# Kernel optimization log

Measured on AMD Instinct MI355X. Metric: run time of the kernel, lower is better.

## Reference

```python
import jax, jax.numpy as jnp
import numpy as np

NUM_HEADS = 4
CATEGORY_SIZE = 128
DIM = 192
B, N, M = 2, 65000, 64


def setup_inputs() -> dict:
    key = jax.random.key(0)
    k1, k2, k3, k4 = jax.random.split(key, 4)
    qkv = jax.random.normal(k1, (B, N, 3 * DIM), dtype=jnp.float32)
    sim = jax.random.normal(k2, (B, N, M), dtype=jnp.float32)
    proj_w = jax.random.normal(k3, (DIM, DIM), dtype=jnp.float32) * (1.0 / np.sqrt(DIM))
    proj_b = jax.random.normal(k4, (DIM,), dtype=jnp.float32) * 0.01
    logit_scale = jnp.log(10.0 * jnp.ones((1, 1), dtype=jnp.float32))
    return {"qkv": qkv, "sim": sim, "proj_w": proj_w, "proj_b": proj_b,
            "logit_scale": logit_scale, "x_size": 65000}


def reference(qkv, sim, proj_w, proj_b, logit_scale, x_size):
    b, n, c3 = qkv.shape
    c = c3 // 3
    h = NUM_HEADS
    gs = min(n, CATEGORY_SIZE)
    ng = (n + gs - 1) // gs
    pad_n = ng * gs - n

    # token -> category id, then sort tokens by category
    tk_id = jnp.argmax(sim, axis=-1)                      # (b, n) int
    sort_idx = jnp.argsort(tk_id, axis=-1)                # (b, n)
    inv_idx = jnp.argsort(sort_idx, axis=-1)              # inverse permutation

    shuffled = jnp.take_along_axis(qkv, sort_idx[..., None], axis=1)  # (b, n, 3c)
    if pad_n > 0:
        pad = jnp.flip(shuffled[:, n - pad_n:n, :], axis=1)
        shuffled = jnp.concatenate([shuffled, pad], axis=1)           # (b, n+pad_n, 3c)

    # (3, b, ng, h, gs, c/h)
    y = shuffled.reshape(b, ng, gs, 3, h, c // h).transpose(3, 0, 1, 4, 2, 5)
    q, k, v = y[0], y[1], y[2]

    scale = jnp.exp(jnp.minimum(logit_scale, jnp.log(jnp.asarray(100.0, dtype=qkv.dtype))))
    attn = jnp.einsum('bghqd,bghkd->bghqk', q, k) * scale  # (b, ng, h, gs, gs)
    attn = jax.nn.softmax(attn, axis=-1)
    out = jnp.einsum('bghqk,bghkd->bghqd', attn, v)        # (b, ng, h, gs, c/h)
    out = out.transpose(0, 1, 3, 2, 4).reshape(b, n + pad_n, c)[:, :n, :]

    # scatter back to original token order
    out = jnp.take_along_axis(out, inv_idx[..., None], axis=1)
    return out @ proj_w.T + proj_b
```

## Files before the change

### kernel.cpp

```cpp
#include <hip/hip_runtime.h>
#include <hip/hip_bf16.h>
#include <math.h>

#define BB 2
#define NN 65000
#define MM 64
#define DIM 192
#define NH 4
#define HD 48
#define GS 128
#define NG 508
#define SORT_TPB 256
#define NBLK 254

#define NROWS_PAD 130048
#define NROWTILES 2032

typedef __attribute__((ext_vector_type(8))) short bf16x8;
typedef __attribute__((ext_vector_type(8))) _Float16 f16x8;
typedef __attribute__((ext_vector_type(2))) __fp16 fp16x2;
typedef __attribute__((ext_vector_type(4))) float f32x4;
typedef __attribute__((ext_vector_type(16))) float f32x16;
typedef __attribute__((ext_vector_type(8))) unsigned short u16x8;

__device__ __forceinline__ unsigned short f2bf(float f) {
  __hip_bfloat16 h = __float2bfloat16(f);
  return *(unsigned short*)&h;
}
__device__ __forceinline__ unsigned int pkh(float lo, float hi) {
  fp16x2 t = __builtin_amdgcn_cvt_pkrtz(lo, hi);
  return *(unsigned int*)&t;
}
__device__ __forceinline__ f16x8 cvt8h(float4 a, float4 b) {
  f16x8 r;
  r[0] = (_Float16)a.x; r[1] = (_Float16)a.y; r[2] = (_Float16)a.z; r[3] = (_Float16)a.w;
  r[4] = (_Float16)b.x; r[5] = (_Float16)b.y; r[6] = (_Float16)b.z; r[7] = (_Float16)b.w;
  return r;
}
__device__ __forceinline__ void gload_lds16(const float* src, float* lds_dst) {
  __builtin_amdgcn_global_load_lds(
      (const __attribute__((address_space(1))) unsigned int*)src,
      (__attribute__((address_space(3))) unsigned int*)lds_dst, 16, 0, 0);
}

__global__ void k_argmax_hist(const float* __restrict__ sim, int* __restrict__ tk,
                              int* __restrict__ hist) {
  __shared__ int cnt[MM];
  const int b = blockIdx.y, blk = blockIdx.x;
  if (threadIdx.x < MM) cnt[threadIdx.x] = 0;
  __syncthreads();
  int t = blk * SORT_TPB + threadIdx.x;
  if (t < NN) {
    const float4* row = (const float4*)(sim + ((size_t)b * NN + t) * MM);
    float best = -INFINITY;
    int bi = 0;
#pragma unroll
    for (int j = 0; j < MM / 4; ++j) {
      float4 v = row[j];
      if (v.x > best) { best = v.x; bi = 4 * j + 0; }
      if (v.y > best) { best = v.y; bi = 4 * j + 1; }
      if (v.z > best) { best = v.z; bi = 4 * j + 2; }
      if (v.w > best) { best = v.w; bi = 4 * j + 3; }
    }
    tk[b * NN + t] = bi;
    atomicAdd(&cnt[bi], 1);
  }
  __syncthreads();
  if (threadIdx.x < MM)
    hist[(b * NBLK + blk) * MM + threadIdx.x] = cnt[threadIdx.x];
}

__global__ void k_scan(const int* __restrict__ hist, int* __restrict__ boff) {
  const int b = blockIdx.x;
  const int tid = threadIdx.x;
  const int seg = tid >> 6, bin = tid & 63;
  __shared__ int part[4][MM];
  __shared__ int basev[MM];
  const int lo = seg * 64, hi = (seg == 3) ? NBLK : (lo + 64);
  int s = 0;
  for (int blk = lo; blk < hi; ++blk) s += hist[(b * NBLK + blk) * MM + bin];
  part[seg][bin] = s;
  __syncthreads();
  if (tid < 64) {
    int tot = part[0][bin] + part[1][bin] + part[2][bin] + part[3][bin];
    int incl = tot;
#pragma unroll
    for (int d = 1; d < 64; d <<= 1) {
      int o = __shfl_up(incl, d);
      if (bin >= d) incl += o;
    }
    basev[bin] = incl - tot;
  }
  __syncthreads();
  int run = basev[bin];
  for (int s2 = 0; s2 < seg; ++s2) run += part[s2][bin];
  for (int blk = lo; blk < hi; ++blk) {
    int h = hist[(b * NBLK + blk) * MM + bin];
    boff[(b * NBLK + blk) * MM + bin] = run;
    run += h;
  }
}

__global__ void k_scatter(const int* __restrict__ tk, const int* __restrict__ boff,
                          int* __restrict__ sidx) {
  __shared__ int sbin[SORT_TPB];
  const int b = blockIdx.y, blk = blockIdx.x;
  int t = blk * SORT_TPB + threadIdx.x;
  int bin = (t < NN) ? tk[b * NN + t] : -1;
  sbin[threadIdx.x] = bin;
  __syncthreads();
  if (t < NN) {
    int rank = 0;
    for (int j = 0; j < (int)threadIdx.x; ++j) rank += (sbin[j] == bin);
    int pos = boff[(b * NBLK + blk) * MM + bin] + rank;
    sidx[b * NN + pos] = t;
  }
}

__global__ __launch_bounds__(256) void k_attn_mfma(const float* __restrict__ qkv,
                                                   const int* __restrict__ sidx,
                                                   const float* __restrict__ logit_scale,
                                                   __hip_bfloat16* __restrict__ attn_out) {
  const int x = blockIdx.x;
  const int g = ((x >> 5) << 3) + (x & 7);
  const int hd = (x >> 3) & 3;
  const int b = blockIdx.z;
  if (g >= NG) return;

  __shared__ int stok[GS];
  __shared__ _Float16 akv[4 * 3 * 64 * 8];
  __shared__ float vrowf[GS][HD];
  __shared__ _Float16 vfrag[2 * 8 * 64 * 8];

  const int tid = threadIdx.x;
  const int w = tid >> 6, l = tid & 63;
  const int hl = l >> 5, l31 = l & 31;

  if (tid < GS) {
    int s = g * GS + tid;
    int sp = (s < NN) ? s : (2 * NN - 1 - s);
    stok[tid] = sidx[b * NN + sp];
  }
  __syncthreads();

#pragma unroll
  for (int i = 0; i < 6; ++i) {
    int c = (i * 4 + w) * 64 + l;
    int row = c / 12, piece = c % 12;
    const float* src = qkv + (size_t)(b * NN + stok[row]) * (3 * DIM) + 2 * DIM + hd * HD + piece * 4;
    gload_lds16(src, &vrowf[0][0] + (i * 4 + w) * 256);
  }

  f16x8 qf[3];
  {
    const float* qsrc = qkv + (size_t)(b * NN + stok[w * 32 + l31]) * (3 * DIM) + hd * HD;
#pragma unroll
    for (int s = 0; s < 3; ++s) {
      const float4* p = (const float4*)(qsrc + s * 16 + hl * 8);
      qf[s] = cvt8h(p[0], p[1]);
    }
  }

#pragma unroll
  for (int i = 0; i < 3; ++i) {
    int c = tid + 256 * i;
    int ts = c >> 6, cl = c & 63;
    int kvr = (ts / 3) * 32 + (cl & 31);
    int dbase = (ts % 3) * 16 + (cl >> 5) * 8;
    const float* src = qkv + (size_t)(b * NN + stok[kvr]) * (3 * DIM) + DIM + hd * HD + dbase;
    ((f16x8*)akv)[c] = cvt8h(((const float4*)src)[0], ((const float4*)src)[1]);
  }
  __syncthreads();

#pragma unroll
  for (int i = 0; i < 4; ++i) {
    int c = tid + 256 * i;
    int ntks = c >> 6, cl = c & 63;
    int nt = ntks >> 3, ks = ntks & 7;
    int d = nt * 32 + (cl & 31);
    int kvb = ks * 16 + (cl >> 5) * 8;
    _Float16 tmp[8];
#pragma unroll
    for (int e = 0; e < 8; ++e) tmp[e] = (d < HD) ? (_Float16)vrowf[kvb + e][d] : (_Float16)0.f;
    ((f16x8*)vfrag)[c] = *(f16x8*)tmp;
  }
  __syncthreads();

  f32x16 accS[4];
#pragma unroll
  for (int t = 0; t < 4; ++t)
#pragma unroll
    for (int r = 0; r < 16; ++r) accS[t][r] = 0.f;

#pragma unroll
  for (int t = 0; t < 4; ++t)
#pragma unroll
    for (int s = 0; s < 3; ++s) {
      f16x8 af = ((const f16x8*)akv)[(t * 3 + s) * 64 + l];
      accS[t] = __builtin_amdgcn_mfma_f32_32x32x16_f16(af, qf[s], accS[t], 0, 0, 0);
    }

  const float scale = expf(fminf(logit_scale[0], 4.6051701860f));
  float mx = -INFINITY;
#pragma unroll
  for (int t = 0; t < 4; ++t)
#pragma unroll
    for (int r = 0; r < 16; ++r) { accS[t][r] *= scale; mx = fmaxf(mx, accS[t][r]); }
  mx = fmaxf(mx, __shfl_xor(mx, 32));
  float sum = 0.f;
#pragma unroll
  for (int t = 0; t < 4; ++t)
#pragma unroll
    for (int r = 0; r < 16; ++r) { float p = __expf(accS[t][r] - mx); accS[t][r] = p; sum += p; }
  sum += __shfl_xor(sum, 32);
  const float inv = 1.f / sum;
#pragma unroll
  for (int t = 0; t < 4; ++t)
#pragma unroll
    for (int r = 0; r < 16; ++r) accS[t][r] *= inv;

  f32x16 accO[2];
#pragma unroll
  for (int nt = 0; nt < 2; ++nt)
#pragma unroll
    for (int r = 0; r < 16; ++r) accO[nt][r] = 0.f;

#pragma unroll
  for (int t = 0; t < 4; ++t) {
    union { unsigned int u[4]; f16x8 v; } fa, fb;
    {
      unsigned int a0 = pkh(accS[t][0], accS[t][1]);
      unsigned int a1 = pkh(accS[t][2], accS[t][3]);
      unsigned int b0 = pkh(accS[t][4], accS[t][5]);
      unsigned int b1 = pkh(accS[t][6], accS[t][7]);
      unsigned int sa0 = __shfl_xor(a0, 32), sa1 = __shfl_xor(a1, 32);
      unsigned int sb0 = __shfl_xor(b0, 32), sb1 = __shfl_xor(b1, 32);
      fa.u[0] = hl ? sb0 : a0; fa.u[1] = hl ? sb1 : a1;
      fa.u[2] = hl ? b0 : sa0; fa.u[3] = hl ? b1 : sa1;
    }
    {
      unsigned int a0 = pkh(accS[t][8], accS[t][9]);
      unsigned int a1 = pkh(accS[t][10], accS[t][11]);
      unsigned int b0 = pkh(accS[t][12], accS[t][13]);
      unsigned int b1 = pkh(accS[t][14], accS[t][15]);
      unsigned int sa0 = __shfl_xor(a0, 32), sa1 = __shfl_xor(a1, 32);
      unsigned int sb0 = __shfl_xor(b0, 32), sb1 = __shfl_xor(b1, 32);
      fb.u[0] = hl ? sb0 : a0; fb.u[1] = hl ? sb1 : a1;
      fb.u[2] = hl ? b0 : sa0; fb.u[3] = hl ? b1 : sa1;
    }
    accO[0] = __builtin_amdgcn_mfma_f32_32x32x16_f16(fa.v, ((const f16x8*)vfrag)[(0 * 8 + 2 * t) * 64 + l], accO[0], 0, 0, 0);
    accO[1] = __builtin_amdgcn_mfma_f32_32x32x16_f16(fa.v, ((const f16x8*)vfrag)[(1 * 8 + 2 * t) * 64 + l], accO[1], 0, 0, 0);
    accO[0] = __builtin_amdgcn_mfma_f32_32x32x16_f16(fb.v, ((const f16x8*)vfrag)[(0 * 8 + 2 * t + 1) * 64 + l], accO[0], 0, 0, 0);
    accO[1] = __builtin_amdgcn_mfma_f32_32x32x16_f16(fb.v, ((const f16x8*)vfrag)[(1 * 8 + 2 * t + 1) * 64 + l], accO[1], 0, 0, 0);
  }

#pragma unroll
  for (int r = 0; r < 16; ++r) {
    int rowl = w * 32 + (r & 3) + 8 * (r >> 2) + 4 * hl;
    int sg = g * GS + rowl;
    if (sg < NN) {
      size_t base = (size_t)(b * NN + stok[rowl]) * DIM + hd * HD;
      attn_out[base + l31] = __float2bfloat16(accO[0][r]);
      if (l31 < 16) attn_out[base + 32 + l31] = __float2bfloat16(accO[1][r]);
    }
  }
}

__global__ void k_wpack(const float* __restrict__ W, unsigned short* __restrict__ wpack) {
  int idx = blockIdx.x * blockDim.x + threadIdx.x;
  if (idx >= 12 * 6 * 64) return;
  int lane = idx & 63;
  int kkjt = idx >> 6;
  int kk = kkjt % 6;
  int jt = kkjt / 6;
  int j = jt * 16 + (lane & 15);
  int k0 = kk * 32 + (lane >> 4) * 8;
  const float* src = W + (size_t)j * DIM + k0;
  unsigned short tmp[8];
#pragma unroll
  for (int e = 0; e < 8; ++e) tmp[e] = f2bf(src[e]);
  ((u16x8*)wpack)[idx] = *(const u16x8*)tmp;
}

__global__ __launch_bounds__(256) void k_proj_mfma(const unsigned short* __restrict__ xb,
                                                   const unsigned short* __restrict__ wpack,
                                                   const float* __restrict__ bias,
                                                   float* __restrict__ out) {
  __shared__ unsigned short wl[6 * 6 * 64 * 8];
  const int tid = threadIdx.x;
  const int jhalf = blockIdx.y;

  const u16x8* wsrc = (const u16x8*)(wpack + (size_t)jhalf * 6 * 6 * 64 * 8);
  for (int i = tid; i < 6 * 6 * 64; i += 256) ((u16x8*)wl)[i] = wsrc[i];
  __syncthreads();

  const int wid = tid >> 6, lane = tid & 63;
  const int l15 = lane & 15, lk = lane >> 4;

  float bv[6];
#pragma unroll
  for (int jt = 0; jt < 6; ++jt) bv[jt] = bias[jhalf * 96 + jt * 16 + l15];

  for (int tile = blockIdx.x; tile < NROWTILES; tile += gridDim.x) {
    const int r0 = tile * 64 + wid * 16;
    f32x4 acc[6];
#pragma unroll
    for (int jt = 0; jt < 6; ++jt) { f32x4 t = {bv[jt], bv[jt], bv[jt], bv[jt]}; acc[jt] = t; }

    const unsigned short* xrow = xb + (size_t)(r0 + l15) * DIM;
#pragma unroll
    for (int kk = 0; kk < 6; ++kk) {
      bf16x8 a = *(const bf16x8*)(xrow + kk * 32 + lk * 8);
#pragma unroll
      for (int jt = 0; jt < 6; ++jt) {
        bf16x8 b = *(const bf16x8*)(wl + ((jt * 6 + kk) * 64 + lane) * 8);
        acc[jt] = __builtin_amdgcn_mfma_f32_16x16x32_bf16(a, b, acc[jt], 0, 0, 0);
      }
    }

    const int rowb = r0 + lk * 4;
#pragma unroll
    for (int jt = 0; jt < 6; ++jt) {
#pragma unroll
      for (int r = 0; r < 4; ++r) {
        int row = rowb + r;
        if (row < BB * NN)
          out[(size_t)row * DIM + jhalf * 96 + jt * 16 + l15] = acc[jt][r];
      }
    }
  }
}

extern "C" void kernel_launch(void* const* d_in, const int* in_sizes, int n_in,
                              void* d_out, int out_size, void* d_ws, size_t ws_size,
                              hipStream_t stream) {
  const float* qkv = (const float*)d_in[0];
  const float* sim = (const float*)d_in[1];
  const float* proj_w = (const float*)d_in[2];
  const float* proj_b = (const float*)d_in[3];
  const float* logit_scale = (const float*)d_in[4];

  unsigned short* x_bf16 = (unsigned short*)d_ws;
  unsigned short* wpack = x_bf16 + (size_t)NROWS_PAD * DIM;
  int* tk = (int*)(wpack + 12 * 6 * 64 * 8);
  int* hist = tk + (size_t)BB * NN;
  int* boff = hist + (size_t)BB * NBLK * MM;
  int* sidx = boff + (size_t)BB * NBLK * MM;

  k_argmax_hist<<<dim3(NBLK, BB), SORT_TPB, 0, stream>>>(sim, tk, hist);
  k_scan<<<BB, 256, 0, stream>>>(hist, boff);
  k_scatter<<<dim3(NBLK, BB), SORT_TPB, 0, stream>>>(tk, boff, sidx);
  k_wpack<<<(12 * 6 * 64 + 255) / 256, 256, 0, stream>>>(proj_w, wpack);
  k_attn_mfma<<<dim3(2048, 1, BB), 256, 0, stream>>>(qkv, sidx, logit_scale,
                                                     (__hip_bfloat16*)x_bf16);
  k_proj_mfma<<<dim3(1016, 2), 256, 0, stream>>>(x_bf16, wpack, proj_b, (float*)d_out);
}
```

Before: 161.7 us.

## Use ballot-based ranking in scatter and full-width output tiles in projection

The scatter kernel now computes each token's stable rank within its bin with wave ballots over the six bin bits plus per-wave histograms in shared memory. This replaces the quadratic shared-memory scan. The projection kernel now has each block compute all 192 output columns, so the bf16 activation rows are read once instead of twice. The whole packed weight matrix is loaded into LDS with direct global-to-LDS loads. The cost is more LDS per block and 12 accumulators per wave, which may lower occupancy.

```diff
diff --git a/kernel.cpp b/kernel.cpp
--- a/kernel.cpp
+++ b/kernel.cpp
@@ -103,15 +103,28 @@
 
 __global__ void k_scatter(const int* __restrict__ tk, const int* __restrict__ boff,
                           int* __restrict__ sidx) {
-  __shared__ int sbin[SORT_TPB];
+  __shared__ int whist[4][MM];
   const int b = blockIdx.y, blk = blockIdx.x;
-  int t = blk * SORT_TPB + threadIdx.x;
+  const int tid = threadIdx.x;
+  const int w = tid >> 6, lane = tid & 63;
+  ((int*)whist)[tid] = 0;
+  __syncthreads();
+  int t = blk * SORT_TPB + tid;
   int bin = (t < NN) ? tk[b * NN + t] : -1;
-  sbin[threadIdx.x] = bin;
-  __syncthreads();
-  if (t < NN) {
-    int rank = 0;
-    for (int j = 0; j < (int)threadIdx.x; ++j) rank += (sbin[j] == bin);
+  unsigned long long m = ~0ull;
+#pragma unroll
+  for (int bit = 0; bit < 6; ++bit) {
+    unsigned long long bl = __ballot((bin >> bit) & 1);
+    m &= ((bin >> bit) & 1) ? bl : ~bl;
+  }
+  int rank_w = __popcll(m & ((1ull << lane) - 1ull));
+  if (bin >= 0 && rank_w == 0) whist[w][bin] = __popcll(m);
+  __syncthreads();
+  if (bin >= 0) {
+    int rank = rank_w;
+#pragma unroll
+    for (int w2 = 0; w2 < 3; ++w2)
+      if (w2 < w) rank += whist[w2][bin];
     int pos = boff[(b * NBLK + blk) * MM + bin] + rank;
     sidx[b * NN + pos] = t;
   }
@@ -286,33 +299,36 @@
                                                    const unsigned short* __restrict__ wpack,
                                                    const float* __restrict__ bias,
                                                    float* __restrict__ out) {
-  __shared__ unsigned short wl[6 * 6 * 64 * 8];
+  __shared__ unsigned short wl[12 * 6 * 64 * 8];
   const int tid = threadIdx.x;
-  const int jhalf = blockIdx.y;
-
-  const u16x8* wsrc = (const u16x8*)(wpack + (size_t)jhalf * 6 * 6 * 64 * 8);
-  for (int i = tid; i < 6 * 6 * 64; i += 256) ((u16x8*)wl)[i] = wsrc[i];
-  __syncthreads();
+
+#pragma unroll
+  for (int j = 0; j < 18; ++j) {
+    int c = j * 256 + tid;
+    gload_lds16((const float*)((const u16x8*)wpack + c), (float*)((u16x8*)wl + c));
+  }
 
   const int wid = tid >> 6, lane = tid & 63;
   const int l15 = lane & 15, lk = lane >> 4;
 
-  float bv[6];
-#pragma unroll
-  for (int jt = 0; jt < 6; ++jt) bv[jt] = bias[jhalf * 96 + jt * 16 + l15];
+  float bv[12];
+#pragma unroll
+  for (int jt = 0; jt < 12; ++jt) bv[jt] = bias[jt * 16 + l15];
+
+  __syncthreads();
 
   for (int tile = blockIdx.x; tile < NROWTILES; tile += gridDim.x) {
     const int r0 = tile * 64 + wid * 16;
-    f32x4 acc[6];
-#pragma unroll
-    for (int jt = 0; jt < 6; ++jt) { f32x4 t = {bv[jt], bv[jt], bv[jt], bv[jt]}; acc[jt] = t; }
+    f32x4 acc[12];
+#pragma unroll
+    for (int jt = 0; jt < 12; ++jt) { f32x4 t = {bv[jt], bv[jt], bv[jt], bv[jt]}; acc[jt] = t; }
 
     const unsigned short* xrow = xb + (size_t)(r0 + l15) * DIM;
 #pragma unroll
     for (int kk = 0; kk < 6; ++kk) {
       bf16x8 a = *(const bf16x8*)(xrow + kk * 32 + lk * 8);
 #pragma unroll
-      for (int jt = 0; jt < 6; ++jt) {
+      for (int jt = 0; jt < 12; ++jt) {
         bf16x8 b = *(const bf16x8*)(wl + ((jt * 6 + kk) * 64 + lane) * 8);
         acc[jt] = __builtin_amdgcn_mfma_f32_16x16x32_bf16(a, b, acc[jt], 0, 0, 0);
       }
@@ -320,12 +336,12 @@
 
     const int rowb = r0 + lk * 4;
 #pragma unroll
-    for (int jt = 0; jt < 6; ++jt) {
+    for (int jt = 0; jt < 12; ++jt) {
 #pragma unroll
       for (int r = 0; r < 4; ++r) {
         int row = rowb + r;
         if (row < BB * NN)
-          out[(size_t)row * DIM + jhalf * 96 + jt * 16 + l15] = acc[jt][r];
+          out[(size_t)row * DIM + jt * 16 + l15] = acc[jt][r];
       }
     }
   }
@@ -353,5 +369,5 @@
   k_wpack<<<(12 * 6 * 64 + 255) / 256, 256, 0, stream>>>(proj_w, wpack);
   k_attn_mfma<<<dim3(2048, 1, BB), 256, 0, stream>>>(qkv, sidx, logit_scale,
                                                      (__hip_bfloat16*)x_bf16);
-  k_proj_mfma<<<dim3(1016, 2), 256, 0, stream>>>(x_bf16, wpack, proj_b, (float*)d_out);
-}
+  k_proj_mfma<<<dim3(1016), 256, 0, stream>>>(x_bf16, wpack, proj_b, (float*)d_out);
+}
```

After: 160.1 us. About the same (-1.0%).
